# Performance work log

Measured on AMD Instinct MI355X. Metric: run time of the kernel, lower is better.

The kernel has to match this reference:

```python
import jax, jax.numpy as jnp
import numpy as np

# dims
B, T, N, D = 4, 256, 64, 512
H, DH = 8, 64            # n_head, d_head; H*DH == D
DF = 4 * D               # SwiGLU hidden
EPS = 1e-6


def rmsnorm(x, w):
    return x * jax.lax.rsqrt(jnp.mean(x * x, axis=-1, keepdims=True) + EPS) * w


def phi(x):
    # positive feature map for kernelized (linear) attention ('SMReg' assumed elu+1 style)
    return jax.nn.elu(x) + 1.0


def heads(x):
    return x.reshape(*x.shape[:-1], H, DH)


def lin_att(Xq, Xkv, wq, wk, wv, wo):
    # low-rank high-order linear attention: kernelized attention applied
    # independently along each tensor mode (time T, entities N), averaged.
    q = phi(heads(Xq @ wq))   # [B,T,N,H,DH]
    k = phi(heads(Xkv @ wk))
    v = heads(Xkv @ wv)
    # mode 1 (time): attend over T, batch over (B,N)
    kv_t = jnp.einsum('btnhk,btnhv->bnhkv', k, v)          # [B,N,H,DH,DH]
    ks_t = k.sum(axis=1)                                   # [B,N,H,DH]
    den_t = jnp.einsum('btnhk,bnhk->btnh', q, ks_t) + EPS
    out_t = jnp.einsum('btnhk,bnhkv->btnhv', q, kv_t) / den_t[..., None]
    # mode 2 (entities): attend over N, batch over (B,T)
    kv_n = jnp.einsum('btnhk,btnhv->bthkv', k, v)
    ks_n = k.sum(axis=2)
    den_n = jnp.einsum('btnhk,bthk->btnh', q, ks_n) + EPS
    out_n = jnp.einsum('btnhk,bthkv->btnhv', q, kv_n) / den_n[..., None]
    out = 0.5 * (out_t + out_n)
    return out.reshape(*Xq.shape[:-1], H * DH) @ wo


def swiglu(x, w1, w2, w3):
    return (jax.nn.silu(x @ w1) * (x @ w3)) @ w2


def setup_inputs() -> dict:
    key = jax.random.key(0)
    ks = jax.random.split(key, 20)
    s = 0.02
    inp = {
        'X': jax.random.normal(ks[0], (B, T, N, D), jnp.float32),
        'Z': jax.random.normal(ks[1], (B, T, N, D), jnp.float32),
        'n1': jnp.ones((D,), jnp.float32),
        'n2': jnp.ones((D,), jnp.float32),
        'n3': jnp.ones((D,), jnp.float32),
        'nz': jnp.ones((D,), jnp.float32),
        'a_wq': jax.random.normal(ks[2], (D, H * DH), jnp.float32) * s,
        'a_wk': jax.random.normal(ks[3], (D, H * DH), jnp.float32) * s,
        'a_wv': jax.random.normal(ks[4], (D, H * DH), jnp.float32) * s,
        'a_wo': jax.random.normal(ks[5], (H * DH, D), jnp.float32) * s,
        'c_wq': jax.random.normal(ks[6], (D, H * DH), jnp.float32) * s,
        'c_wk': jax.random.normal(ks[7], (D, H * DH), jnp.float32) * s,
        'c_wv': jax.random.normal(ks[8], (D, H * DH), jnp.float32) * s,
        'c_wo': jax.random.normal(ks[9], (H * DH, D), jnp.float32) * s,
        'f_w1': jax.random.normal(ks[10], (D, DF), jnp.float32) * s,
        'f_w2': jax.random.normal(ks[11], (DF, D), jnp.float32) * s,
        'f_w3': jax.random.normal(ks[12], (D, DF), jnp.float32) * s,
    }
    return inp


def reference(X, Z, n1, n2, n3, nz, a_wq, a_wk, a_wv, a_wo,
              c_wq, c_wk, c_wv, c_wo, f_w1, f_w2, f_w3):
    # h = X + SelfAtt(norm1(X))
    xn = rmsnorm(X, n1)
    h = X + lin_att(xn, xn, a_wq, a_wk, a_wv, a_wo)
    # h = h + CrossAtt(norm3(h), normz(Z))
    h = h + lin_att(rmsnorm(h, n3), rmsnorm(Z, nz), c_wq, c_wk, c_wv, c_wo)
    # out = h + SwiGLU(norm2(h))   (dropout p=0 -> identity)
    return h + swiglu(rmsnorm(h, n2), f_w1, f_w2, f_w3)
```

## Files before the change

kernel.cpp:

```cpp
#include <hip/hip_runtime.h>

typedef short s16x8 __attribute__((ext_vector_type(8)));
typedef float f32x4 __attribute__((ext_vector_type(4)));
typedef unsigned short u16;
typedef unsigned int u32;

__device__ __forceinline__ float bf2f(u16 u) {
  union { unsigned int i; float f; } v; v.i = ((unsigned int)u) << 16; return v.f;
}
__device__ __forceinline__ u16 f2bf(float f) {
  union { float f; unsigned int i; } v; v.f = f;
  unsigned int r = v.i + 0x7fffu + ((v.i >> 16) & 1u);
  return (u16)(r >> 16);
}

__device__ __forceinline__ void gload16(const u16* g, u16* l) {
  __builtin_amdgcn_global_load_lds(
      (const __attribute__((address_space(1))) u32*)g,
      (__attribute__((address_space(3))) u32*)l, 16, 0, 0);
}

template<int KDIM, int NDIM>
__launch_bounds__(256)
__global__ void wprep(const float* __restrict__ in, u16* __restrict__ out) {
  __shared__ float t[64][65];
  const int tid = threadIdx.x;
  const int nb = NDIM / 64;
  const int tk0 = (blockIdx.x / nb) * 64;
  const int tn0 = (blockIdx.x % nb) * 64;
#pragma unroll
  for (int i = 0; i < 16; i++) {
    int idx = i * 256 + tid;
    int r = idx >> 6, c = idx & 63;
    t[r][c] = in[(long)(tk0 + r) * NDIM + (tn0 + c)];
  }
  __syncthreads();
#pragma unroll
  for (int i = 0; i < 16; i++) {
    int idx = i * 256 + tid;
    int nn = idx >> 6, kk = idx & 63;
    out[(long)(tn0 + nn) * KDIM + (tk0 + kk)] = f2bf(t[kk][nn]);
  }
}

__launch_bounds__(256)
__global__ void rmsnorm_f32(const float* __restrict__ x, const float* __restrict__ w,
                            u16* __restrict__ out) {
  const long row = (long)blockIdx.x * 4 + (threadIdx.x >> 6);
  const int lane = threadIdx.x & 63;
  const float* xr = x + row * 512 + lane * 8;
  float4 v0 = *(const float4*)xr;
  float4 v1 = *(const float4*)(xr + 4);
  float ss = v0.x*v0.x + v0.y*v0.y + v0.z*v0.z + v0.w*v0.w
           + v1.x*v1.x + v1.y*v1.y + v1.z*v1.z + v1.w*v1.w;
#pragma unroll
  for (int o = 1; o < 64; o <<= 1) ss += __shfl_xor(ss, o);
  float sc = rsqrtf(ss * (1.0f / 512.0f) + 1e-6f);
  const float* wp = w + lane * 8;
  float4 w0 = *(const float4*)wp;
  float4 w1 = *(const float4*)(wp + 4);
  union { u16 u[8]; uint4 v; } o;
  o.u[0] = f2bf(v0.x * sc * w0.x);
  o.u[1] = f2bf(v0.y * sc * w0.y);
  o.u[2] = f2bf(v0.z * sc * w0.z);
  o.u[3] = f2bf(v0.w * sc * w0.w);
  o.u[4] = f2bf(v1.x * sc * w1.x);
  o.u[5] = f2bf(v1.y * sc * w1.y);
  o.u[6] = f2bf(v1.z * sc * w1.z);
  o.u[7] = f2bf(v1.w * sc * w1.w);
  *(uint4*)(out + row * 512 + lane * 8) = o.v;
}

__launch_bounds__(256)
__global__ void rmsnorm_bf16(const u16* __restrict__ x, const float* __restrict__ w,
                             u16* __restrict__ out) {
  const long row = (long)blockIdx.x * 4 + (threadIdx.x >> 6);
  const int lane = threadIdx.x & 63;
  uint4 u = *(const uint4*)(x + row * 512 + lane * 8);
  const u16* us = (const u16*)&u;
  float f[8];
  float ss = 0.f;
#pragma unroll
  for (int j = 0; j < 8; j++) { f[j] = bf2f(us[j]); ss += f[j] * f[j]; }
#pragma unroll
  for (int o = 1; o < 64; o <<= 1) ss += __shfl_xor(ss, o);
  float sc = rsqrtf(ss * (1.0f / 512.0f) + 1e-6f);
  const float* wp = w + lane * 8;
  union { u16 u[8]; uint4 v; } o;
#pragma unroll
  for (int j = 0; j < 8; j++) o.u[j] = f2bf(f[j] * sc * wp[j]);
  *(uint4*)(out + row * 512 + lane * 8) = o.v;
}

enum { EPI_BF16 = 0, EPI_PHI = 1, EPI_RESX = 2, EPI_RESH = 3, EPI_SILUMUL = 4, EPI_OUTF = 5 };

template<int KD, int EPI>
__launch_bounds__(512)
__global__ void gemm256(const u16* __restrict__ A, const u16* __restrict__ Bt,
                        void* __restrict__ Cout, const void* __restrict__ aux,
                        int Ns) {
  __shared__ u16 As[2][256][64];
  __shared__ u16 Bs[2][256][64];
  const int tid = threadIdx.x;
  const int lane = tid & 63;
  const int wid = tid >> 6;
  const int gx = gridDim.x;
  int L = blockIdx.y * gx + blockIdx.x;
  const int cpx = (gx * gridDim.y) >> 3;
  L = (L & 7) * cpx + (L >> 3);
  const long m0 = (long)(L / gx) * 256;
  const long n0 = (long)(L % gx) * 256;

  const int wrbase = (wid >> 2) * 128;
  const int wcbase = (wid & 3) * 64;
  const int fr = lane & 15;
  const int frq = lane >> 4;

  const int rA0 = wid * 8 + (lane >> 3);
  const int sg8 = (((lane & 7) ^ ((lane >> 3) & 7))) * 8;
  const u16* Ag = A + (m0 + rA0) * KD + sg8;
  const u16* Bg = Bt + (n0 + rA0) * KD + sg8;
  u16* Alds = &As[0][0][0] + wid * 512;
  u16* Blds = &Bs[0][0][0] + wid * 512;

  f32x4 acc[8][4] = {};

  auto STAGE = [&](int b, int kt) {
    const long k0 = (long)kt * 64;
#pragma unroll
    for (int j = 0; j < 4; j++) {
      gload16(Ag + (long)(j * 64) * KD + k0, Alds + b * 16384 + j * 4096);
      gload16(Bg + (long)(j * 64) * KD + k0, Blds + b * 16384 + j * 4096);
    }
  };
  auto COMPUTE = [&](int b) {
#pragma unroll
    for (int ks = 0; ks < 2; ks++) {
      const int slot = ((ks * 4 + frq) ^ (fr & 7)) * 8;
      s16x8 af[8], bf[4];
#pragma unroll
      for (int i = 0; i < 8; i++) af[i] = *(const s16x8*)&As[b][wrbase + i * 16 + fr][slot];
#pragma unroll
      for (int j = 0; j < 4; j++) bf[j] = *(const s16x8*)&Bs[b][wcbase + j * 16 + fr][slot];
#pragma unroll
      for (int i = 0; i < 8; i++)
#pragma unroll
        for (int j = 0; j < 4; j++)
          acc[i][j] = __builtin_amdgcn_mfma_f32_16x16x32_bf16(af[i], bf[j], acc[i][j], 0, 0, 0);
    }
  };

  constexpr int NT = KD / 64;
  STAGE(0, 0);
#pragma unroll 1
  for (int t = 0; t < NT; ++t) {
    if (t + 1 < NT) {
      STAGE((t + 1) & 1, t + 1);
      asm volatile("s_waitcnt vmcnt(8)" ::: "memory");
    } else {
      asm volatile("s_waitcnt vmcnt(0)" ::: "memory");
    }
    __builtin_amdgcn_s_barrier();
    COMPUTE(t & 1);
    asm volatile("s_waitcnt lgkmcnt(0)" ::: "memory");
    __builtin_amdgcn_s_barrier();
  }

  const int col = lane & 15;
  const int rb = frq * 4;
#pragma unroll
  for (int i = 0; i < 8; i++) {
#pragma unroll
    for (int r = 0; r < 4; r++) {
      long m = m0 + wrbase + i * 16 + rb + r;
#pragma unroll
      for (int j = 0; j < 4; j++) {
        long n = n0 + wcbase + j * 16 + col;
        long off = m * Ns + n;
        float v = acc[i][j][r];
        if constexpr (EPI == EPI_BF16) {
          ((u16*)Cout)[off] = f2bf(v);
        } else if constexpr (EPI == EPI_PHI) {
          float p = v > 0.f ? v + 1.f : __expf(v);
          ((u16*)Cout)[off] = f2bf(p);
        } else if constexpr (EPI == EPI_RESX) {
          ((u16*)Cout)[off] = f2bf(((const float*)aux)[off] + v);
        } else if constexpr (EPI == EPI_RESH) {
          ((u16*)Cout)[off] = f2bf(bf2f(((const u16*)aux)[off]) + v);
        } else if constexpr (EPI == EPI_SILUMUL) {
          float t2 = bf2f(((const u16*)aux)[off]);
          float s = t2 / (1.f + __expf(-t2));
          ((u16*)Cout)[off] = f2bf(s * v);
        } else {
          ((float*)Cout)[off] = bf2f(((const u16*)aux)[off]) + v;
        }
      }
    }
  }
}

__launch_bounds__(256)
__global__ void att_mode1(const u16* __restrict__ q, const u16* __restrict__ k,
                          const u16* __restrict__ v, u16* __restrict__ attc) {
  __shared__ u16 Ks[128][72];
  __shared__ u16 Vs[128][72];
  __shared__ u16 KVT[64][72];
  __shared__ float ksump[4][64];
  __shared__ float ksum_s[64];
  __shared__ float dinv[256];
  const int tid = threadIdx.x;
  const int lane = tid & 63;
  const int w = tid >> 6;
  const int bnh = blockIdx.x;
  const int h = bnh & 7;
  const int bn = bnh >> 3;
  const int n = bn & 63;
  const int b = bn >> 6;
  const long base = ((long)b * 16384 + n) * 512 + h * 64;
  const int fr = lane & 15;
  const int fk = (lane >> 4) * 8;
  const int sdk = tid & 63, sqq = tid >> 6;

  f32x4 acc[4] = {};
  float ks_acc = 0.f;

  for (int half = 0; half < 2; half++) {
    __syncthreads();
#pragma unroll
    for (int rep = 0; rep < 4; rep++) {
      int idx = rep * 256 + tid;
      int tl = idx >> 3, c8 = idx & 7;
      long go = base + (long)(half * 128 + tl) * 32768 + c8 * 8;
      *(uint4*)&Ks[tl][c8 * 8] = *(const uint4*)(k + go);
      *(uint4*)&Vs[tl][c8 * 8] = *(const uint4*)(v + go);
    }
    __syncthreads();
#pragma unroll
    for (int i = 0; i < 32; i++) ks_acc += bf2f(Ks[sqq * 32 + i][sdk]);
#pragma unroll
    for (int ks = 0; ks < 4; ks++) {
      s16x8 af, bfr[4];
#pragma unroll
      for (int e = 0; e < 8; e++) af[e] = (short)Vs[ks * 32 + fk + e][w * 16 + fr];
#pragma unroll
      for (int j = 0; j < 4; j++)
#pragma unroll
        for (int e = 0; e < 8; e++) bfr[j][e] = (short)Ks[ks * 32 + fk + e][j * 16 + fr];
#pragma unroll
      for (int j = 0; j < 4; j++)
        acc[j] = __builtin_amdgcn_mfma_f32_16x16x32_bf16(af, bfr[j], acc[j], 0, 0, 0);
    }
  }
  ksump[sqq][sdk] = ks_acc;
  __syncthreads();
  {
    const int colL = lane & 15, rb = (lane >> 4) * 4;
#pragma unroll
    for (int j = 0; j < 4; j++)
#pragma unroll
      for (int r = 0; r < 4; r++)
        KVT[w * 16 + rb + r][j * 16 + colL] = f2bf(acc[j][r]);
  }
  if (tid < 64) ksum_s[tid] = ksump[0][tid] + ksump[1][tid] + ksump[2][tid] + ksump[3][tid];
  __syncthreads();
  {
    const u16* qp = q + base + (long)tid * 32768;
    float d = 0.f;
#pragma unroll
    for (int c8 = 0; c8 < 8; c8++) {
      uint4 u = ((const uint4*)qp)[c8];
      const u16* us = (const u16*)&u;
#pragma unroll
      for (int e = 0; e < 8; e++) d += bf2f(us[e]) * ksum_s[c8 * 8 + e];
    }
    dinv[tid] = 0.5f / (d + 1e-6f);
  }
  f32x4 acc2[4][4] = {};
#pragma unroll
  for (int ks = 0; ks < 2; ks++) {
    s16x8 aq[4], bk[4];
#pragma unroll
    for (int i = 0; i < 4; i++)
      aq[i] = *(const s16x8*)(q + base + (long)(w * 64 + i * 16 + fr) * 32768 + ks * 32 + fk);
#pragma unroll
    for (int j = 0; j < 4; j++)
      bk[j] = *(const s16x8*)&KVT[j * 16 + fr][ks * 32 + fk];
#pragma unroll
    for (int i = 0; i < 4; i++)
#pragma unroll
      for (int j = 0; j < 4; j++)
        acc2[i][j] = __builtin_amdgcn_mfma_f32_16x16x32_bf16(aq[i], bk[j], acc2[i][j], 0, 0, 0);
  }
  __syncthreads();
  const int colL = lane & 15, rb = (lane >> 4) * 4;
#pragma unroll
  for (int i = 0; i < 4; i++)
#pragma unroll
    for (int r = 0; r < 4; r++) {
      int t = w * 64 + i * 16 + rb + r;
      float inv = dinv[t];
#pragma unroll
      for (int j = 0; j < 4; j++)
        attc[base + (long)t * 32768 + j * 16 + colL] = f2bf(acc2[i][j][r] * inv);
    }
}

__launch_bounds__(256)
__global__ void att_mode2(const u16* __restrict__ q, const u16* __restrict__ k,
                          const u16* __restrict__ v, u16* __restrict__ attc) {
  __shared__ u16 Ks[64][72];
  __shared__ u16 Vs[64][72];
  __shared__ u16 KVT[64][72];
  __shared__ float ksump[4][64];
  __shared__ float ksum_s[64];
  __shared__ float dinv[64];
  const int tid = threadIdx.x;
  const int lane = tid & 63;
  const int w = tid >> 6;
  const int bth = blockIdx.x;
  const int h = bth & 7;
  const long bt = bth >> 3;
  const long base = bt * 32768 + h * 64;
  const int fr = lane & 15;
  const int fk = (lane >> 4) * 8;
  const int sdk = tid & 63, sqq = tid >> 6;

#pragma unroll
  for (int rep = 0; rep < 2; rep++) {
    int idx = rep * 256 + tid;
    int nl = idx >> 3, c8 = idx & 7;
    long go = base + (long)nl * 512 + c8 * 8;
    *(uint4*)&Ks[nl][c8 * 8] = *(const uint4*)(k + go);
    *(uint4*)&Vs[nl][c8 * 8] = *(const uint4*)(v + go);
  }
  __syncthreads();
  {
    float s = 0.f;
#pragma unroll
    for (int i = 0; i < 16; i++) s += bf2f(Ks[sqq * 16 + i][sdk]);
    ksump[sqq][sdk] = s;
  }
  f32x4 acc[4] = {};
#pragma unroll
  for (int ks = 0; ks < 2; ks++) {
    s16x8 af, bfr[4];
#pragma unroll
    for (int e = 0; e < 8; e++) af[e] = (short)Vs[ks * 32 + fk + e][w * 16 + fr];
#pragma unroll
    for (int j = 0; j < 4; j++)
#pragma unroll
      for (int e = 0; e < 8; e++) bfr[j][e] = (short)Ks[ks * 32 + fk + e][j * 16 + fr];
#pragma unroll
    for (int j = 0; j < 4; j++)
      acc[j] = __builtin_amdgcn_mfma_f32_16x16x32_bf16(af, bfr[j], acc[j], 0, 0, 0);
  }
  __syncthreads();
  {
    const int colL = lane & 15, rb = (lane >> 4) * 4;
#pragma unroll
    for (int j = 0; j < 4; j++)
#pragma unroll
      for (int r = 0; r < 4; r++)
        KVT[w * 16 + rb + r][j * 16 + colL] = f2bf(acc[j][r]);
  }
  if (tid < 64) ksum_s[tid] = ksump[0][tid] + ksump[1][tid] + ksump[2][tid] + ksump[3][tid];
  __syncthreads();
  if (tid < 64) {
    const u16* qp = q + base + (long)tid * 512;
    float d = 0.f;
#pragma unroll
    for (int c8 = 0; c8 < 8; c8++) {
      uint4 u = ((const uint4*)qp)[c8];
      const u16* us = (const u16*)&u;
#pragma unroll
      for (int e = 0; e < 8; e++) d += bf2f(us[e]) * ksum_s[c8 * 8 + e];
    }
    dinv[tid] = 0.5f / (d + 1e-6f);
  }
  f32x4 acc2[4] = {};
#pragma unroll
  for (int ks = 0; ks < 2; ks++) {
    s16x8 aq, bk[4];
    aq = *(const s16x8*)(q + base + (long)(w * 16 + fr) * 512 + ks * 32 + fk);
#pragma unroll
    for (int j = 0; j < 4; j++)
      bk[j] = *(const s16x8*)&KVT[j * 16 + fr][ks * 32 + fk];
#pragma unroll
    for (int j = 0; j < 4; j++)
      acc2[j] = __builtin_amdgcn_mfma_f32_16x16x32_bf16(aq, bk[j], acc2[j], 0, 0, 0);
  }
  __syncthreads();
  const int colL = lane & 15, rb = (lane >> 4) * 4;
#pragma unroll
  for (int r = 0; r < 4; r++) {
    int nr = w * 16 + rb + r;
    float inv = dinv[nr];
#pragma unroll
    for (int j = 0; j < 4; j++) {
      long o = base + (long)nr * 512 + j * 16 + colL;
      attc[o] = f2bf(bf2f(attc[o]) + acc2[j][r] * inv);
    }
  }
}

extern "C" void kernel_launch(void* const* d_in, const int* in_sizes, int n_in,
                              void* d_out, int out_size, void* d_ws, size_t ws_size,
                              hipStream_t stream) {
  const float* X    = (const float*)d_in[0];
  const float* Z    = (const float*)d_in[1];
  const float* n1   = (const float*)d_in[2];
  const float* n2   = (const float*)d_in[3];
  const float* n3   = (const float*)d_in[4];
  const float* nz   = (const float*)d_in[5];
  const float* a_wq = (const float*)d_in[6];
  const float* a_wk = (const float*)d_in[7];
  const float* a_wv = (const float*)d_in[8];
  const float* a_wo = (const float*)d_in[9];
  const float* c_wq = (const float*)d_in[10];
  const float* c_wk = (const float*)d_in[11];
  const float* c_wv = (const float*)d_in[12];
  const float* c_wo = (const float*)d_in[13];
  const float* f_w1 = (const float*)d_in[14];
  const float* f_w2 = (const float*)d_in[15];
  const float* f_w3 = (const float*)d_in[16];
  float* out = (float*)d_out;
  (void)ws_size; (void)in_sizes; (void)n_in; (void)out_size;

  char* p = (char*)d_ws;
  size_t off = 0;
  auto take = [&](size_t bytes) -> char* {
    char* r = p + off;
    off += (bytes + 255) & ~(size_t)255;
    return r;
  };
  u16* w_aq = (u16*)take(512 * 512 * 2);
  u16* w_ak = (u16*)take(512 * 512 * 2);
  u16* w_av = (u16*)take(512 * 512 * 2);
  u16* w_ao = (u16*)take(512 * 512 * 2);
  u16* w_cq = (u16*)take(512 * 512 * 2);
  u16* w_ck = (u16*)take(512 * 512 * 2);
  u16* w_cv = (u16*)take(512 * 512 * 2);
  u16* w_co = (u16*)take(512 * 512 * 2);
  u16* w_f1 = (u16*)take(2048 * 512 * 2);
  u16* w_f3 = (u16*)take(2048 * 512 * 2);
  u16* w_f2 = (u16*)take(512 * 2048 * 2);
  u16* xn   = (u16*)take((size_t)65536 * 512 * 2);
  u16* hbuf = (u16*)take((size_t)65536 * 512 * 2);
  u16* qbuf = (u16*)take((size_t)65536 * 512 * 2);
  u16* kbuf = (u16*)d_out;
  u16* vbuf = (u16*)d_out + (size_t)65536 * 512;
  u16* attc = xn;
  u16* tslot = qbuf;

  dim3 b256(256);
  dim3 b512(512);
  dim3 gP(2, 256);
  dim3 gU(8, 64);
  dim3 gD(2, 64);

  wprep<512, 512><<<64, b256, 0, stream>>>(a_wq, w_aq);
  wprep<512, 512><<<64, b256, 0, stream>>>(a_wk, w_ak);
  wprep<512, 512><<<64, b256, 0, stream>>>(a_wv, w_av);
  wprep<512, 512><<<64, b256, 0, stream>>>(a_wo, w_ao);
  wprep<512, 512><<<64, b256, 0, stream>>>(c_wq, w_cq);
  wprep<512, 512><<<64, b256, 0, stream>>>(c_wk, w_ck);
  wprep<512, 512><<<64, b256, 0, stream>>>(c_wv, w_cv);
  wprep<512, 512><<<64, b256, 0, stream>>>(c_wo, w_co);
  wprep<512, 2048><<<256, b256, 0, stream>>>(f_w1, w_f1);
  wprep<512, 2048><<<256, b256, 0, stream>>>(f_w3, w_f3);
  wprep<2048, 512><<<256, b256, 0, stream>>>(f_w2, w_f2);

  rmsnorm_f32<<<16384, b256, 0, stream>>>(X, n1, xn);
  gemm256<512, EPI_PHI><<<gP, b512, 0, stream>>>(xn, w_aq, qbuf, nullptr, 512);
  gemm256<512, EPI_PHI><<<gP, b512, 0, stream>>>(xn, w_ak, kbuf, nullptr, 512);
  gemm256<512, EPI_BF16><<<gP, b512, 0, stream>>>(xn, w_av, vbuf, nullptr, 512);
  att_mode1<<<2048, b256, 0, stream>>>(qbuf, kbuf, vbuf, attc);
  att_mode2<<<8192, b256, 0, stream>>>(qbuf, kbuf, vbuf, attc);
  gemm256<512, EPI_RESX><<<gP, b512, 0, stream>>>(attc, w_ao, hbuf, X, 512);

  rmsnorm_bf16<<<16384, b256, 0, stream>>>(hbuf, n3, xn);
  gemm256<512, EPI_PHI><<<gP, b512, 0, stream>>>(xn, w_cq, qbuf, nullptr, 512);
  rmsnorm_f32<<<16384, b256, 0, stream>>>(Z, nz, xn);
  gemm256<512, EPI_PHI><<<gP, b512, 0, stream>>>(xn, w_ck, kbuf, nullptr, 512);
  gemm256<512, EPI_BF16><<<gP, b512, 0, stream>>>(xn, w_cv, vbuf, nullptr, 512);
  att_mode1<<<2048, b256, 0, stream>>>(qbuf, kbuf, vbuf, attc);
  att_mode2<<<8192, b256, 0, stream>>>(qbuf, kbuf, vbuf, attc);
  gemm256<512, EPI_RESH><<<gP, b512, 0, stream>>>(attc, w_co, hbuf, hbuf, 512);

  rmsnorm_bf16<<<16384, b256, 0, stream>>>(hbuf, n2, xn);
  const int CH = 16384;
  for (int c = 0; c < 4; c++) {
    const size_t ro = (size_t)c * CH * 512;
    gemm256<512, EPI_BF16><<<gU, b512, 0, stream>>>(xn + ro, w_f1, tslot, nullptr, 2048);
    gemm256<512, EPI_SILUMUL><<<gU, b512, 0, stream>>>(xn + ro, w_f3, tslot, tslot, 2048);
    gemm256<2048, EPI_OUTF><<<gD, b512, 0, stream>>>(tslot, w_f2, out + ro, hbuf + ro, 512);
  }
}
```

Measured before the change: 1.565 ms.

## Shrink GEMM tiles to 128x128 and fuse Q/K/V projections into one GEMM

The 256x256 GEMM with 512 threads is replaced by a 128x128 tile GEMM with 256 threads, and all launch grids are resized to match. The self-attention Q, K and V projections become a single GEMM over the concatenated weight matrices, and the cross-attention K and V projections become another. A segment-aware epilogue routes each column block to its output buffer and applies phi only to Q and K. This cuts kernel launches, reads the normalized activations once per fused GEMM, and raises the block count for occupancy. In exchange, smaller tiles reuse each loaded operand less, and the fusion depends on the prepared weight buffers being laid out contiguously.

```diff
diff --git a/kernel.cpp b/kernel.cpp
--- a/kernel.cpp
+++ b/kernel.cpp
@@ -92,58 +92,61 @@
   *(uint4*)(out + row * 512 + lane * 8) = o.v;
 }
 
-enum { EPI_BF16 = 0, EPI_PHI = 1, EPI_RESX = 2, EPI_RESH = 3, EPI_SILUMUL = 4, EPI_OUTF = 5 };
+enum { EPI_BF16 = 0, EPI_PHI = 1, EPI_RESX = 2, EPI_RESH = 3, EPI_SILUMUL = 4,
+       EPI_OUTF = 5, EPI_QKV = 6, EPI_KV = 7 };
 
 template<int KD, int EPI>
-__launch_bounds__(512)
-__global__ void gemm256(const u16* __restrict__ A, const u16* __restrict__ Bt,
-                        void* __restrict__ Cout, const void* __restrict__ aux,
+__launch_bounds__(256)
+__global__ void gemm128(const u16* __restrict__ A, const u16* __restrict__ Bt,
+                        void* __restrict__ C0, void* __restrict__ C1,
+                        void* __restrict__ C2, const void* __restrict__ aux,
                         int Ns) {
-  __shared__ u16 As[2][256][64];
-  __shared__ u16 Bs[2][256][64];
+  __shared__ u16 As[2][128][64];
+  __shared__ u16 Bs[2][128][64];
   const int tid = threadIdx.x;
   const int lane = tid & 63;
-  const int wid = tid >> 6;
+  const int wv = tid >> 6;
   const int gx = gridDim.x;
   int L = blockIdx.y * gx + blockIdx.x;
   const int cpx = (gx * gridDim.y) >> 3;
   L = (L & 7) * cpx + (L >> 3);
-  const long m0 = (long)(L / gx) * 256;
-  const long n0 = (long)(L % gx) * 256;
-
-  const int wrbase = (wid >> 2) * 128;
-  const int wcbase = (wid & 3) * 64;
+  const long m0 = (long)(L / gx) * 128;
+  const int nb = L % gx;
+  const long n0 = (long)nb * 128;
+
+  const int wr = (wv >> 1) * 64;
+  const int wc = (wv & 1) * 64;
   const int fr = lane & 15;
   const int frq = lane >> 4;
 
-  const int rA0 = wid * 8 + (lane >> 3);
-  const int sg8 = (((lane & 7) ^ ((lane >> 3) & 7))) * 8;
-  const u16* Ag = A + (m0 + rA0) * KD + sg8;
-  const u16* Bg = Bt + (n0 + rA0) * KD + sg8;
-  u16* Alds = &As[0][0][0] + wid * 512;
-  u16* Blds = &Bs[0][0][0] + wid * 512;
-
-  f32x4 acc[8][4] = {};
+  const int r0 = wv * 32 + (lane >> 3);
+  const int sg8 = ((lane & 7) ^ ((lane >> 3) & 7)) * 8;
+  const u16* Ag = A + (m0 + r0) * KD + sg8;
+  const u16* Bg = Bt + (n0 + r0) * KD + sg8;
+  u16* Alds = &As[0][0][0] + wv * 2048;
+  u16* Blds = &Bs[0][0][0] + wv * 2048;
+
+  f32x4 acc[4][4] = {};
 
   auto STAGE = [&](int b, int kt) {
     const long k0 = (long)kt * 64;
 #pragma unroll
     for (int j = 0; j < 4; j++) {
-      gload16(Ag + (long)(j * 64) * KD + k0, Alds + b * 16384 + j * 4096);
-      gload16(Bg + (long)(j * 64) * KD + k0, Blds + b * 16384 + j * 4096);
+      gload16(Ag + (long)(j * 8) * KD + k0, Alds + b * 8192 + j * 512);
+      gload16(Bg + (long)(j * 8) * KD + k0, Blds + b * 8192 + j * 512);
     }
   };
   auto COMPUTE = [&](int b) {
 #pragma unroll
     for (int ks = 0; ks < 2; ks++) {
       const int slot = ((ks * 4 + frq) ^ (fr & 7)) * 8;
-      s16x8 af[8], bf[4];
-#pragma unroll
-      for (int i = 0; i < 8; i++) af[i] = *(const s16x8*)&As[b][wrbase + i * 16 + fr][slot];
-#pragma unroll
-      for (int j = 0; j < 4; j++) bf[j] = *(const s16x8*)&Bs[b][wcbase + j * 16 + fr][slot];
-#pragma unroll
-      for (int i = 0; i < 8; i++)
+      s16x8 af[4], bf[4];
+#pragma unroll
+      for (int i = 0; i < 4; i++) af[i] = *(const s16x8*)&As[b][wr + i * 16 + fr][slot];
+#pragma unroll
+      for (int j = 0; j < 4; j++) bf[j] = *(const s16x8*)&Bs[b][wc + j * 16 + fr][slot];
+#pragma unroll
+      for (int i = 0; i < 4; i++)
 #pragma unroll
         for (int j = 0; j < 4; j++)
           acc[i][j] = __builtin_amdgcn_mfma_f32_16x16x32_bf16(af[i], bf[j], acc[i][j], 0, 0, 0);
@@ -169,30 +172,44 @@
   const int col = lane & 15;
   const int rb = frq * 4;
 #pragma unroll
-  for (int i = 0; i < 8; i++) {
+  for (int i = 0; i < 4; i++) {
 #pragma unroll
     for (int r = 0; r < 4; r++) {
-      long m = m0 + wrbase + i * 16 + rb + r;
+      long m = m0 + wr + i * 16 + rb + r;
 #pragma unroll
       for (int j = 0; j < 4; j++) {
-        long n = n0 + wcbase + j * 16 + col;
-        long off = m * Ns + n;
+        long nlocal = wc + j * 16 + col;
         float v = acc[i][j][r];
-        if constexpr (EPI == EPI_BF16) {
-          ((u16*)Cout)[off] = f2bf(v);
-        } else if constexpr (EPI == EPI_PHI) {
-          float p = v > 0.f ? v + 1.f : __expf(v);
-          ((u16*)Cout)[off] = f2bf(p);
-        } else if constexpr (EPI == EPI_RESX) {
-          ((u16*)Cout)[off] = f2bf(((const float*)aux)[off] + v);
-        } else if constexpr (EPI == EPI_RESH) {
-          ((u16*)Cout)[off] = f2bf(bf2f(((const u16*)aux)[off]) + v);
-        } else if constexpr (EPI == EPI_SILUMUL) {
-          float t2 = bf2f(((const u16*)aux)[off]);
-          float s = t2 / (1.f + __expf(-t2));
-          ((u16*)Cout)[off] = f2bf(s * v);
+        if constexpr (EPI == EPI_QKV) {
+          int seg = nb >> 2;
+          long off = m * 512 + ((n0 + nlocal) & 511);
+          u16* P = (u16*)(seg == 0 ? C0 : (seg == 1 ? C1 : C2));
+          float p = (seg < 2) ? (v > 0.f ? v + 1.f : __expf(v)) : v;
+          P[off] = f2bf(p);
+        } else if constexpr (EPI == EPI_KV) {
+          int seg = nb >> 2;
+          long off = m * 512 + ((n0 + nlocal) & 511);
+          u16* P = (u16*)(seg == 0 ? C0 : C1);
+          float p = (seg == 0) ? (v > 0.f ? v + 1.f : __expf(v)) : v;
+          P[off] = f2bf(p);
         } else {
-          ((float*)Cout)[off] = bf2f(((const u16*)aux)[off]) + v;
+          long off = m * Ns + (n0 + nlocal);
+          if constexpr (EPI == EPI_BF16) {
+            ((u16*)C0)[off] = f2bf(v);
+          } else if constexpr (EPI == EPI_PHI) {
+            float p = v > 0.f ? v + 1.f : __expf(v);
+            ((u16*)C0)[off] = f2bf(p);
+          } else if constexpr (EPI == EPI_RESX) {
+            ((u16*)C0)[off] = f2bf(((const float*)aux)[off] + v);
+          } else if constexpr (EPI == EPI_RESH) {
+            ((u16*)C0)[off] = f2bf(bf2f(((const u16*)aux)[off]) + v);
+          } else if constexpr (EPI == EPI_SILUMUL) {
+            float t2 = bf2f(((const u16*)aux)[off]);
+            float s = t2 / (1.f + __expf(-t2));
+            ((u16*)C0)[off] = f2bf(s * v);
+          } else {
+            ((float*)C0)[off] = bf2f(((const u16*)aux)[off]) + v;
+          }
         }
       }
     }
@@ -453,10 +470,11 @@
   u16* tslot = qbuf;
 
   dim3 b256(256);
-  dim3 b512(512);
-  dim3 gP(2, 256);
-  dim3 gU(8, 64);
-  dim3 gD(2, 64);
+  dim3 gQKV(12, 512);
+  dim3 gKV(8, 512);
+  dim3 gP(4, 512);
+  dim3 gU(16, 128);
+  dim3 gD(4, 128);
 
   wprep<512, 512><<<64, b256, 0, stream>>>(a_wq, w_aq);
   wprep<512, 512><<<64, b256, 0, stream>>>(a_wk, w_ak);
@@ -471,28 +489,25 @@
   wprep<2048, 512><<<256, b256, 0, stream>>>(f_w2, w_f2);
 
   rmsnorm_f32<<<16384, b256, 0, stream>>>(X, n1, xn);
-  gemm256<512, EPI_PHI><<<gP, b512, 0, stream>>>(xn, w_aq, qbuf, nullptr, 512);
-  gemm256<512, EPI_PHI><<<gP, b512, 0, stream>>>(xn, w_ak, kbuf, nullptr, 512);
-  gemm256<512, EPI_BF16><<<gP, b512, 0, stream>>>(xn, w_av, vbuf, nullptr, 512);
+  gemm128<512, EPI_QKV><<<gQKV, b256, 0, stream>>>(xn, w_aq, qbuf, kbuf, vbuf, nullptr, 1536);
   att_mode1<<<2048, b256, 0, stream>>>(qbuf, kbuf, vbuf, attc);
   att_mode2<<<8192, b256, 0, stream>>>(qbuf, kbuf, vbuf, attc);
-  gemm256<512, EPI_RESX><<<gP, b512, 0, stream>>>(attc, w_ao, hbuf, X, 512);
+  gemm128<512, EPI_RESX><<<gP, b256, 0, stream>>>(attc, w_ao, hbuf, nullptr, nullptr, X, 512);
 
   rmsnorm_bf16<<<16384, b256, 0, stream>>>(hbuf, n3, xn);
-  gemm256<512, EPI_PHI><<<gP, b512, 0, stream>>>(xn, w_cq, qbuf, nullptr, 512);
+  gemm128<512, EPI_PHI><<<gP, b256, 0, stream>>>(xn, w_cq, qbuf, nullptr, nullptr, nullptr, 512);
   rmsnorm_f32<<<16384, b256, 0, stream>>>(Z, nz, xn);
-  gemm256<512, EPI_PHI><<<gP, b512, 0, stream>>>(xn, w_ck, kbuf, nullptr, 512);
-  gemm256<512, EPI_BF16><<<gP, b512, 0, stream>>>(xn, w_cv, vbuf, nullptr, 512);
+  gemm128<512, EPI_KV><<<gKV, b256, 0, stream>>>(xn, w_ck, kbuf, vbuf, nullptr, nullptr, 1024);
   att_mode1<<<2048, b256, 0, stream>>>(qbuf, kbuf, vbuf, attc);
   att_mode2<<<8192, b256, 0, stream>>>(qbuf, kbuf, vbuf, attc);
-  gemm256<512, EPI_RESH><<<gP, b512, 0, stream>>>(attc, w_co, hbuf, hbuf, 512);
+  gemm128<512, EPI_RESH><<<gP, b256, 0, stream>>>(attc, w_co, hbuf, nullptr, nullptr, hbuf, 512);
 
   rmsnorm_bf16<<<16384, b256, 0, stream>>>(hbuf, n2, xn);
   const int CH = 16384;
   for (int c = 0; c < 4; c++) {
     const size_t ro = (size_t)c * CH * 512;
-    gemm256<512, EPI_BF16><<<gU, b512, 0, stream>>>(xn + ro, w_f1, tslot, nullptr, 2048);
-    gemm256<512, EPI_SILUMUL><<<gU, b512, 0, stream>>>(xn + ro, w_f3, tslot, tslot, 2048);
-    gemm256<2048, EPI_OUTF><<<gD, b512, 0, stream>>>(tslot, w_f2, out + ro, hbuf + ro, 512);
-  }
-}
+    gemm128<512, EPI_BF16><<<gU, b256, 0, stream>>>(xn + ro, w_f1, tslot, nullptr, nullptr, nullptr, 2048);
+    gemm128<512, EPI_SILUMUL><<<gU, b256, 0, stream>>>(xn + ro, w_f3, tslot, nullptr, nullptr, tslot, 2048);
+    gemm128<2048, EPI_OUTF><<<gD, b256, 0, stream>>>(tslot, w_f2, out + ro, nullptr, nullptr, hbuf + ro, 512);
+  }
+}
```

After: 1.498 ms. 1.04x faster.
